# Optimization experiments

Measured on AMD Instinct MI355X. Metric: run time of the kernel, lower is better.

The kernel has to match this reference:

```python
import jax, jax.numpy as jnp
import numpy as np

BLOCK_SIZES = [256] * 16
LAYER_SIZE = sum(BLOCK_SIZES)  # 4096
N_ROWS = 8192


def _block_diag_mask(sizes):
    m = np.zeros((sum(sizes), sum(sizes)), dtype=bool)
    off = 0
    for s in sizes:
        m[off:off + s, off:off + s] = True
        off += s
    return jnp.asarray(m)


def setup_inputs() -> dict:
    key = jax.random.key(0)
    k1, k2 = jax.random.split(key)
    mask = _block_diag_mask(BLOCK_SIZES)
    # _blocks param: block_diagonal(raw_blocks) -> dense matrix, zero off-block
    blocks = jax.random.normal(k1, (LAYER_SIZE, LAYER_SIZE), dtype=jnp.float32) * mask
    x = jax.random.normal(k2, (N_ROWS, LAYER_SIZE), dtype=jnp.float32)
    return {"x": x, "blocks": blocks, "mask": mask}


def reference(x, blocks, mask):
    # blocks property: mask then tanh (constrained='tanh'); tanh(0)=0 preserves structure
    b = jnp.tanh(blocks * mask)
    # forward: dense matmul x @ blocks (no bias)
    return x @ b
```

## Files before the change

kernel.cpp:

```cpp
#include <hip/hip_runtime.h>
#include <stdint.h>


typedef float floatx4 __attribute__((ext_vector_type(4)));
typedef __bf16 bf16x8 __attribute__((ext_vector_type(8)));

#define LDX 4096
#define NBLK 16
#define BS 256

__device__ __forceinline__ unsigned int f2bf(float f) {
  union { float f; unsigned int i; } x;
  x.f = f;
  unsigned int r = x.i + 0x7FFFu + ((x.i >> 16) & 1u);
  return r >> 16;
}

__device__ __forceinline__ bf16x8 pack8(const float4& a, const float4& b) {
  union { uint4 u; bf16x8 h; } v;
  v.u.x = f2bf(a.x) | (f2bf(a.y) << 16);
  v.u.y = f2bf(a.z) | (f2bf(a.w) << 16);
  v.u.z = f2bf(b.x) | (f2bf(b.y) << 16);
  v.u.w = f2bf(b.z) | (f2bf(b.w) << 16);
  return v.h;
}

__device__ __forceinline__ void async_copy16(const void* g, void* l) {
  __builtin_amdgcn_global_load_lds(
      (__attribute__((address_space(1))) void*)(uintptr_t)g,
      (__attribute__((address_space(3))) void*)(unsigned int)(uintptr_t)l,
      16, 0, 0);
}

__global__ __launch_bounds__(256) void tanh_pack(const float* __restrict__ blocks,
                                                 unsigned short* __restrict__ wsT) {
  __shared__ float tile[64][65];
  const int t = threadIdx.x;
  const int tc = blockIdx.x, tr = blockIdx.y, j = blockIdx.z;
  const float* src = blocks + (size_t)(j * BS + tr * 64) * LDX + j * BS + tc * 64;
#pragma unroll
  for (int it = 0; it < 8; ++it) {
    int v = it * 256 + t;
    int row = v >> 5;
    int c2 = (v & 31) * 2;
    float2 f = *(const float2*)(src + (size_t)row * LDX + c2);
    tile[row][c2] = tanhf(f.x);
    tile[row][c2 + 1] = tanhf(f.y);
  }
  __syncthreads();
  unsigned char* dstj =
      (unsigned char*)wsT + (size_t)j * 131072 + (size_t)tr * 32768;
#pragma unroll
  for (int it = 0; it < 8; ++it) {
    int v = it * 256 + t;
    int nn = v >> 5;
    int k2 = (v & 31) * 2;
    int n = tc * 64 + nn;
    unsigned int pair = f2bf(tile[k2][nn]) | (f2bf(tile[k2 + 1][nn]) << 16);
    unsigned int off = (unsigned)n * 128 + (((unsigned)(k2 * 2)) ^ (((unsigned)(n & 7)) << 4));
    *(unsigned int*)(dstj + off) = pair;
  }
}

__global__ __launch_bounds__(512, 4) void bdgemm5(const float* __restrict__ x,
                                                  const unsigned short* __restrict__ wsT,
                                                  float* __restrict__ out) {
  __shared__ unsigned short Bs[32768];
  const int t = threadIdx.x;
  const int lane = t & 63;
  const int wave = t >> 6;
  const int bx = blockIdx.x;
  const int mg = bx >> 1;
  const int nh = bx & 1;
  const int j = blockIdx.y;

  const int fr = lane & 15;
  const int kq = lane >> 4;
  const int sw = (fr & 7) << 4;

  char* bsb = (char*)Bs;

  const int row = mg * 128 + wave * 16 + fr;
  const float* ap = x + (size_t)row * LDX + j * BS + kq * 8;

  float4 sa[2][2];
  sa[0][0] = *(const float4*)(ap);
  sa[0][1] = *(const float4*)(ap + 4);
  sa[1][0] = *(const float4*)(ap + 32);
  sa[1][1] = *(const float4*)(ap + 36);

  const char* wsj = (const char*)wsT + (size_t)j * 131072 + nh * 16384;
#pragma unroll
  for (int i = 0; i < 8; ++i) {
    const int c = i >> 1, h = i & 1;
    async_copy16(wsj + c * 32768 + h * 8192 + t * 16,
                 bsb + c * 16384 + h * 8192 + t * 16);
  }
  asm volatile("s_waitcnt vmcnt(0)" ::: "memory");
  __builtin_amdgcn_s_barrier();

  floatx4 acc[8];
#pragma unroll
  for (int b = 0; b < 8; ++b) acc[b] = (floatx4){0.f, 0.f, 0.f, 0.f};

#pragma unroll
  for (int kk = 0; kk < 8; ++kk) {
    const int sl = kk & 1;
    bf16x8 af = pack8(sa[sl][0], sa[sl][1]);
    if (kk + 2 < 8) {
      sa[sl][0] = *(const float4*)(ap + (kk + 2) * 32);
      sa[sl][1] = *(const float4*)(ap + (kk + 2) * 32 + 4);
    }
    const char* bb =
        bsb + (kk >> 1) * 16384 + fr * 128 + (((kk & 1) * 64 + kq * 16) ^ sw);
#pragma unroll
    for (int ni = 0; ni < 8; ++ni) {
      bf16x8 bf = *(const bf16x8*)(bb + ni * 2048);
      acc[ni] = __builtin_amdgcn_mfma_f32_16x16x32_bf16(af, bf, acc[ni], 0, 0, 0);
    }
  }

  float* op0 = out + (size_t)(mg * 128 + wave * 16 + kq * 4) * LDX + j * BS +
               nh * 128 + fr;
#pragma unroll
  for (int ni = 0; ni < 8; ++ni)
#pragma unroll
    for (int r = 0; r < 4; ++r)
      op0[(size_t)r * LDX + ni * 16] = acc[ni][r];
}

template <int BSTR>
__global__ __launch_bounds__(256) void bdgemm_fused(const float* __restrict__ x,
                                                    const float* __restrict__ bg,
                                                    float* __restrict__ out) {
  __shared__ unsigned short As[64 * 32];
  __shared__ unsigned short Bsf[256 * BSTR];
  const int t = threadIdx.x;
  const int lane = t & 63;
  const int wave = t >> 6;
  const int mtile = blockIdx.x;
  const int j = blockIdx.y;
  const int m0 = mtile * 64;
  const float* xg = x + (size_t)m0 * LDX + j * BS;
  const int srow = t >> 2;
  const int scol = (t & 3) * 8;
  const int wn = wave * 64;
  const int fr = lane & 15;
  const int fq = (lane >> 4) * 8;

  floatx4 acc[4][4];
#pragma unroll
  for (int a = 0; a < 4; ++a)
#pragma unroll
    for (int b = 0; b < 4; ++b) acc[a][b] = (floatx4){0.f, 0.f, 0.f, 0.f};

  for (int kt = 0; kt < 8; ++kt) {
    const int k0 = kt * 32;
    const float* ap = xg + (size_t)srow * LDX + k0 + scol;
    float4 a0 = *(const float4*)(ap);
    float4 a1 = *(const float4*)(ap + 4);
    uint4 pk;
    pk.x = f2bf(a0.x) | (f2bf(a0.y) << 16);
    pk.y = f2bf(a0.z) | (f2bf(a0.w) << 16);
    pk.z = f2bf(a1.x) | (f2bf(a1.y) << 16);
    pk.w = f2bf(a1.z) | (f2bf(a1.w) << 16);
    *(uint4*)(As + t * 8) = pk;
#pragma unroll
    for (int i = 0; i < 32; ++i) {
      const int idx = i * 256 + t;
      const int kk = idx >> 8;
      const int nn = idx & 255;
      float v = tanhf(bg[(size_t)(j * BS + k0 + kk) * LDX + j * BS + nn]);
      Bsf[nn * BSTR + kk] = (unsigned short)f2bf(v);
    }
    __syncthreads();
    bf16x8 af[4], bfm[4];
#pragma unroll
    for (int i = 0; i < 4; ++i) {
      af[i] = *(const bf16x8*)(As + (i * 16 + fr) * 32 + fq);
      bfm[i] = *(const bf16x8*)(Bsf + (wn + i * 16 + fr) * BSTR + fq);
    }
#pragma unroll
    for (int mi = 0; mi < 4; ++mi)
#pragma unroll
      for (int ni = 0; ni < 4; ++ni)
        acc[mi][ni] =
            __builtin_amdgcn_mfma_f32_16x16x32_bf16(af[mi], bfm[ni], acc[mi][ni], 0, 0, 0);
    __syncthreads();
  }
  const int r0 = (lane >> 4) * 4;
  const int ocol = j * BS + wn + fr;
#pragma unroll
  for (int mi = 0; mi < 4; ++mi)
#pragma unroll
    for (int ni = 0; ni < 4; ++ni) {
      float* op = out + (size_t)(m0 + mi * 16 + r0) * LDX + ocol + ni * 16;
#pragma unroll
      for (int r = 0; r < 4; ++r) op[(size_t)r * LDX] = acc[mi][ni][r];
    }
}

extern "C" void kernel_launch(void* const* d_in, const int* in_sizes, int n_in,
                              void* d_out, int out_size, void* d_ws, size_t ws_size,
                              hipStream_t stream) {
  const float* x = (const float*)d_in[0];
  const float* blocks = (const float*)d_in[1];
  float* out = (float*)d_out;

  const size_t need = (size_t)NBLK * BS * BS * sizeof(unsigned short);
  if (d_ws != nullptr && ws_size >= need) {
    unsigned short* wsT = (unsigned short*)d_ws;
    tanh_pack<<<dim3(4, 4, NBLK), 256, 0, stream>>>(blocks, wsT);
    bdgemm5<<<dim3(128, NBLK), 512, 0, stream>>>(x, wsT, out);
  } else {
    bdgemm_fused<40><<<dim3(128, NBLK), 256, 0, stream>>>(x, blocks, out);
  }
}
```

Baseline: 331.0 us.

## Load full 256x256 weight block per workgroup and process 512 rows with swapped MFMA operands

Each workgroup now loads the whole bf16 weight block (128KB LDS) once and computes 512 rows in two 256-row passes, instead of 128 rows by half the columns. This amortizes the weight load over more rows, deepens the x prefetch to four stages, and swaps MFMA operands so each lane stores a float4 of contiguous output columns. In exchange the grid drops to 256 workgroups, occupancy falls, and register pressure rises with 32 accumulators per lane.

```diff
diff --git a/kernel.cpp b/kernel.cpp
--- a/kernel.cpp
+++ b/kernel.cpp
@@ -62,16 +62,14 @@
   }
 }
 
-__global__ __launch_bounds__(512, 4) void bdgemm5(const float* __restrict__ x,
+__global__ __launch_bounds__(512, 2) void bdgemm7(const float* __restrict__ x,
                                                   const unsigned short* __restrict__ wsT,
                                                   float* __restrict__ out) {
-  __shared__ unsigned short Bs[32768];
+  __shared__ unsigned short Bs[65536];
   const int t = threadIdx.x;
   const int lane = t & 63;
   const int wave = t >> 6;
-  const int bx = blockIdx.x;
-  const int mg = bx >> 1;
-  const int nh = bx & 1;
+  const int mg = blockIdx.x;
   const int j = blockIdx.y;
 
   const int fr = lane & 15;
@@ -80,53 +78,70 @@
 
   char* bsb = (char*)Bs;
 
-  const int row = mg * 128 + wave * 16 + fr;
-  const float* ap = x + (size_t)row * LDX + j * BS + kq * 8;
-
-  float4 sa[2][2];
-  sa[0][0] = *(const float4*)(ap);
-  sa[0][1] = *(const float4*)(ap + 4);
-  sa[1][0] = *(const float4*)(ap + 32);
-  sa[1][1] = *(const float4*)(ap + 36);
-
-  const char* wsj = (const char*)wsT + (size_t)j * 131072 + nh * 16384;
-#pragma unroll
-  for (int i = 0; i < 8; ++i) {
-    const int c = i >> 1, h = i & 1;
-    async_copy16(wsj + c * 32768 + h * 8192 + t * 16,
-                 bsb + c * 16384 + h * 8192 + t * 16);
-  }
+  const float* ap = x + (size_t)(mg * 512 + wave * 32 + fr) * LDX + j * BS + kq * 8;
+
+  float4 sa[4][4];
+  floatx4 acc[2][16];
+
+  auto issue = [&](int c) {
+    const float* p = ap + (size_t)((c >> 3) * 256) * LDX + (c & 7) * 32;
+    float4* s = sa[c & 3];
+    s[0] = *(const float4*)(p);
+    s[1] = *(const float4*)(p + 4);
+    s[2] = *(const float4*)(p + (size_t)16 * LDX);
+    s[3] = *(const float4*)(p + (size_t)16 * LDX + 4);
+  };
+
+  auto compute = [&](int c) {
+    const float4* s = sa[c & 3];
+    bf16x8 af0 = pack8(s[0], s[1]);
+    bf16x8 af1 = pack8(s[2], s[3]);
+    if (c + 4 < 16) issue(c + 4);
+    const int kk = c & 7;
+    const char* bb =
+        bsb + (kk >> 1) * 32768 + fr * 128 + (((kk & 1) * 64 + kq * 16) ^ sw);
+#pragma unroll
+    for (int ni = 0; ni < 16; ++ni) {
+      bf16x8 bf = *(const bf16x8*)(bb + ni * 2048);
+      acc[0][ni] = __builtin_amdgcn_mfma_f32_16x16x32_bf16(bf, af0, acc[0][ni], 0, 0, 0);
+      acc[1][ni] = __builtin_amdgcn_mfma_f32_16x16x32_bf16(bf, af1, acc[1][ni], 0, 0, 0);
+    }
+  };
+
+  auto zacc = [&]() {
+#pragma unroll
+    for (int a = 0; a < 2; ++a)
+#pragma unroll
+      for (int b = 0; b < 16; ++b) acc[a][b] = (floatx4){0.f, 0.f, 0.f, 0.f};
+  };
+
+  auto storep = [&](int p) {
+    float* op0 = out + (size_t)(mg * 512 + p * 256 + wave * 32 + fr) * LDX +
+                 j * BS + kq * 4;
+#pragma unroll
+    for (int sub = 0; sub < 2; ++sub)
+#pragma unroll
+      for (int ni = 0; ni < 16; ++ni)
+        *(floatx4*)(op0 + (size_t)(sub * 16) * LDX + ni * 16) = acc[sub][ni];
+  };
+
+  const char* wsj = (const char*)wsT + (size_t)j * 131072;
+#pragma unroll
+  for (int i = 0; i < 16; ++i)
+    async_copy16(wsj + i * 8192 + t * 16, bsb + i * 8192 + t * 16);
+  __builtin_amdgcn_sched_barrier(0);
+  issue(0); issue(1); issue(2); issue(3);
   asm volatile("s_waitcnt vmcnt(0)" ::: "memory");
   __builtin_amdgcn_s_barrier();
 
-  floatx4 acc[8];
-#pragma unroll
-  for (int b = 0; b < 8; ++b) acc[b] = (floatx4){0.f, 0.f, 0.f, 0.f};
-
-#pragma unroll
-  for (int kk = 0; kk < 8; ++kk) {
-    const int sl = kk & 1;
-    bf16x8 af = pack8(sa[sl][0], sa[sl][1]);
-    if (kk + 2 < 8) {
-      sa[sl][0] = *(const float4*)(ap + (kk + 2) * 32);
-      sa[sl][1] = *(const float4*)(ap + (kk + 2) * 32 + 4);
-    }
-    const char* bb =
-        bsb + (kk >> 1) * 16384 + fr * 128 + (((kk & 1) * 64 + kq * 16) ^ sw);
-#pragma unroll
-    for (int ni = 0; ni < 8; ++ni) {
-      bf16x8 bf = *(const bf16x8*)(bb + ni * 2048);
-      acc[ni] = __builtin_amdgcn_mfma_f32_16x16x32_bf16(af, bf, acc[ni], 0, 0, 0);
-    }
-  }
-
-  float* op0 = out + (size_t)(mg * 128 + wave * 16 + kq * 4) * LDX + j * BS +
-               nh * 128 + fr;
-#pragma unroll
-  for (int ni = 0; ni < 8; ++ni)
-#pragma unroll
-    for (int r = 0; r < 4; ++r)
-      op0[(size_t)r * LDX + ni * 16] = acc[ni][r];
+  zacc();
+#pragma unroll
+  for (int c = 0; c < 8; ++c) compute(c);
+  storep(0);
+  zacc();
+#pragma unroll
+  for (int c = 8; c < 16; ++c) compute(c);
+  storep(1);
 }
 
 template <int BSTR>
@@ -211,7 +226,7 @@
   if (d_ws != nullptr && ws_size >= need) {
     unsigned short* wsT = (unsigned short*)d_ws;
     tanh_pack<<<dim3(4, 4, NBLK), 256, 0, stream>>>(blocks, wsT);
-    bdgemm5<<<dim3(128, NBLK), 512, 0, stream>>>(x, wsT, out);
+    bdgemm7<<<dim3(16, NBLK), 512, 0, stream>>>(x, wsT, out);
   } else {
     bdgemm_fused<40><<<dim3(128, NBLK), 256, 0, stream>>>(x, blocks, out);
   }
```

After: 308.9 us. -6.7%, faster.

## Read packed weights directly from global, swap MFMA operands for vector stores

Applied to the files above, without the earlier changes.

The GEMM kernel drops the LDS staging of the packed bf16 weight block and has each wave read B fragments straight from global memory (L2-resident). Each workgroup now covers 64 rows by the full 256 columns of a block with 256 threads, holding 16 accumulators per wave. MFMA operands are swapped so each lane owns 4 contiguous output columns, which allows 16-byte vector stores instead of scalar strided stores. The cost is more global/L2 traffic for B, since every wave re-reads it with no LDS reuse, and higher register pressure from 16 accumulators.

```diff
diff --git a/kernel.cpp b/kernel.cpp
--- a/kernel.cpp
+++ b/kernel.cpp
@@ -23,13 +23,6 @@
   v.u.z = f2bf(b.x) | (f2bf(b.y) << 16);
   v.u.w = f2bf(b.z) | (f2bf(b.w) << 16);
   return v.h;
-}
-
-__device__ __forceinline__ void async_copy16(const void* g, void* l) {
-  __builtin_amdgcn_global_load_lds(
-      (__attribute__((address_space(1))) void*)(uintptr_t)g,
-      (__attribute__((address_space(3))) void*)(unsigned int)(uintptr_t)l,
-      16, 0, 0);
 }
 
 __global__ __launch_bounds__(256) void tanh_pack(const float* __restrict__ blocks,
@@ -62,71 +55,51 @@
   }
 }
 
-__global__ __launch_bounds__(512, 4) void bdgemm5(const float* __restrict__ x,
+__global__ __launch_bounds__(256, 4) void bdgemm8(const float* __restrict__ x,
                                                   const unsigned short* __restrict__ wsT,
                                                   float* __restrict__ out) {
-  __shared__ unsigned short Bs[32768];
   const int t = threadIdx.x;
   const int lane = t & 63;
   const int wave = t >> 6;
-  const int bx = blockIdx.x;
-  const int mg = bx >> 1;
-  const int nh = bx & 1;
+  const int rg = blockIdx.x;
   const int j = blockIdx.y;
 
   const int fr = lane & 15;
   const int kq = lane >> 4;
   const int sw = (fr & 7) << 4;
 
-  char* bsb = (char*)Bs;
+  const int row = rg * 64 + wave * 16 + fr;
+  const float* ap = x + (size_t)row * LDX + j * BS + kq * 8;
+  const char* wsj = (const char*)wsT + (size_t)j * 131072 + fr * 128;
 
-  const int row = mg * 128 + wave * 16 + fr;
-  const float* ap = x + (size_t)row * LDX + j * BS + kq * 8;
+  float4 pa[2][2];
+  pa[0][0] = *(const float4*)(ap);
+  pa[0][1] = *(const float4*)(ap + 4);
 
-  float4 sa[2][2];
-  sa[0][0] = *(const float4*)(ap);
-  sa[0][1] = *(const float4*)(ap + 4);
-  sa[1][0] = *(const float4*)(ap + 32);
-  sa[1][1] = *(const float4*)(ap + 36);
-
-  const char* wsj = (const char*)wsT + (size_t)j * 131072 + nh * 16384;
+  floatx4 acc[16];
 #pragma unroll
-  for (int i = 0; i < 8; ++i) {
-    const int c = i >> 1, h = i & 1;
-    async_copy16(wsj + c * 32768 + h * 8192 + t * 16,
-                 bsb + c * 16384 + h * 8192 + t * 16);
-  }
-  asm volatile("s_waitcnt vmcnt(0)" ::: "memory");
-  __builtin_amdgcn_s_barrier();
-
-  floatx4 acc[8];
-#pragma unroll
-  for (int b = 0; b < 8; ++b) acc[b] = (floatx4){0.f, 0.f, 0.f, 0.f};
+  for (int i = 0; i < 16; ++i) acc[i] = (floatx4){0.f, 0.f, 0.f, 0.f};
 
 #pragma unroll
-  for (int kk = 0; kk < 8; ++kk) {
-    const int sl = kk & 1;
-    bf16x8 af = pack8(sa[sl][0], sa[sl][1]);
-    if (kk + 2 < 8) {
-      sa[sl][0] = *(const float4*)(ap + (kk + 2) * 32);
-      sa[sl][1] = *(const float4*)(ap + (kk + 2) * 32 + 4);
+  for (int c = 0; c < 8; ++c) {
+    if (c + 1 < 8) {
+      const float* p = ap + (c + 1) * 32;
+      pa[(c + 1) & 1][0] = *(const float4*)(p);
+      pa[(c + 1) & 1][1] = *(const float4*)(p + 4);
     }
-    const char* bb =
-        bsb + (kk >> 1) * 16384 + fr * 128 + (((kk & 1) * 64 + kq * 16) ^ sw);
+    bf16x8 af = pack8(pa[c & 1][0], pa[c & 1][1]);
+    const char* bb = wsj + (c >> 1) * 32768 + (((c & 1) * 64 + kq * 16) ^ sw);
 #pragma unroll
-    for (int ni = 0; ni < 8; ++ni) {
+    for (int ni = 0; ni < 16; ++ni) {
       bf16x8 bf = *(const bf16x8*)(bb + ni * 2048);
-      acc[ni] = __builtin_amdgcn_mfma_f32_16x16x32_bf16(af, bf, acc[ni], 0, 0, 0);
+      acc[ni] = __builtin_amdgcn_mfma_f32_16x16x32_bf16(bf, af, acc[ni], 0, 0, 0);
     }
   }
 
-  float* op0 = out + (size_t)(mg * 128 + wave * 16 + kq * 4) * LDX + j * BS +
-               nh * 128 + fr;
+  float* op0 = out + (size_t)row * LDX + j * BS + kq * 4;
 #pragma unroll
-  for (int ni = 0; ni < 8; ++ni)
-#pragma unroll
-    for (int r = 0; r < 4; ++r)
-      op0[(size_t)r * LDX + ni * 16] = acc[ni][r];
+  for (int ni = 0; ni < 16; ++ni)
+    *(floatx4*)(op0 + ni * 16) = acc[ni];
 }
 
 template <int BSTR>
@@ -211,7 +184,7 @@
   if (d_ws != nullptr && ws_size >= need) {
     unsigned short* wsT = (unsigned short*)d_ws;
     tanh_pack<<<dim3(4, 4, NBLK), 256, 0, stream>>>(blocks, wsT);
-    bdgemm5<<<dim3(128, NBLK), 512, 0, stream>>>(x, wsT, out);
+    bdgemm8<<<dim3(128, NBLK), 256, 0, stream>>>(x, wsT, out);
   } else {
     bdgemm_fused<40><<<dim3(128, NBLK), 256, 0, stream>>>(x, blocks, out);
   }
```

Measured after the change: 372.8 us. +12.6%, slower.
